# Performance work log

Hardware: AMD Instinct MI355X
Metric: run time of the kernel (lower is better)

The kernel has to match this reference:

```python
import jax, jax.numpy as jnp
import numpy as np

DIM = 1024
NUM_HEADS = 16
HEAD_DIM = DIM // NUM_HEADS
PATCH_SIZE = 20
SHIFT = 2
B, N = 8, 4096


def _patch_index(n, patch_size, shift):
    """Replicates the torch module's static index construction (numpy, host-side)."""
    base = np.arange(0, patch_size * shift, shift, dtype=np.int64)[None, :]  # [1, ps]
    group = np.concatenate([base + i for i in range(shift)], axis=0)        # [shift, ps]
    blocks = [group]
    idx = group
    while idx[-1, -1] < n:
        idx = idx + patch_size * shift
        blocks.append(idx)
    return np.concatenate(blocks, axis=0)  # [R, ps], a permutation of 0..padded-1


PATCH_INDEX = _patch_index(N, PATCH_SIZE, SHIFT)
PAD_SIZE = PATCH_SIZE * SHIFT - N % (PATCH_SIZE * SHIFT)


def setup_inputs() -> dict:
    key = jax.random.key(0)
    k1, k2, k3 = jax.random.split(key, 3)
    x = jax.random.normal(k1, (B, N, DIM), dtype=jnp.float32)
    Wqkv = jax.random.normal(k2, (3 * DIM, DIM), dtype=jnp.float32) * 0.02  # torch Linear weight [out,in]
    Wout = jax.random.normal(k3, (DIM, DIM), dtype=jnp.float32) * 0.02
    bout = jnp.zeros((DIM,), dtype=jnp.float32)
    return {"x": x, "Wqkv": Wqkv, "Wout": Wout, "bout": bout}


def reference(x, Wqkv, Wout, bout):
    Bq, Nq, C = x.shape
    scale = HEAD_DIM ** -0.5
    pidx = jnp.asarray(PATCH_INDEX)                              # [R, S]
    x_pad = jnp.concatenate(
        [x, jnp.zeros((Bq, PAD_SIZE, C), dtype=x.dtype)], axis=1)  # [B, Np, C]
    xp = x_pad[:, pidx, :]                                        # gather -> [B, R, S, C]
    qkv = jnp.einsum('brsc,dc->brsd', xp, Wqkv)                   # [B, R, S, 3C]
    Rr, Sp = pidx.shape
    qkv = qkv.reshape(Bq, Rr, Sp, 3, NUM_HEADS, HEAD_DIM)
    q = qkv[..., 0, :, :].transpose(0, 1, 3, 2, 4)                # [B, R, H, S, hd]
    k = qkv[..., 1, :, :].transpose(0, 1, 3, 2, 4)
    v = qkv[..., 2, :, :].transpose(0, 1, 3, 2, 4)
    dots = jnp.einsum('brhsd,brhtd->brhst', q, k) * scale         # [B, R, H, S, S]
    attn = jax.nn.softmax(dots, axis=-1)                          # dropout: eval mode (identity)
    out = jnp.einsum('brhst,brhtd->brhsd', attn, v)               # [B, R, H, S, hd]
    out = out.transpose(0, 1, 3, 2, 4).reshape(Bq, Rr, Sp, C)
    # scatter back (patch_index is a permutation, so no conflicts)
    x_pad = x_pad.at[:, pidx.reshape(-1), :].set(out.reshape(Bq, -1, C))
    return x_pad[:, :Nq, :] @ Wout.T + bout
```

## Files before the change

### kernel.cpp

```cpp
#include <hip/hip_runtime.h>

#define BQ      8
#define SEQ     4096
#define DIM_    1024
#define QKVD    3072
#define NPATCH  206
#define MTOT    (BQ * SEQ)

typedef __bf16 bf16x8 __attribute__((ext_vector_type(8)));
typedef float  f32x4  __attribute__((ext_vector_type(4)));

__device__ __forceinline__ float bf2f(unsigned int u16) {
  union { unsigned int i; float f; } x;
  x.i = u16 << 16;
  return x.f;
}
__device__ __forceinline__ unsigned short f2bf(float f) {
  union { float f; unsigned int i; } x; x.f = f;
  unsigned int r = x.i + 0x7fffu + ((x.i >> 16) & 1u);
  return (unsigned short)(r >> 16);
}

__device__ __forceinline__ void load_lds16(const void* g, void* l) {
  __builtin_amdgcn_global_load_lds(
      (const __attribute__((address_space(1))) void*)g,
      (__attribute__((address_space(3))) void*)l, 16, 0, 0);
}

__global__ __launch_bounds__(256) void cvt_kernel(
    const float* __restrict__ x,  unsigned short* __restrict__ xb,
    const float* __restrict__ w1, unsigned short* __restrict__ w1b,
    const float* __restrict__ w2, unsigned short* __restrict__ w2b)
{
  const long long NX  = (long long)MTOT * DIM_;
  const long long NW1 = (long long)QKVD * DIM_;
  const long long NW2 = (long long)DIM_ * DIM_;
  const long long total4 = (NX + NW1 + NW2) >> 2;
  for (long long q = (long long)blockIdx.x * 256 + threadIdx.x; q < total4;
       q += (long long)gridDim.x * 256) {
    const float* src; unsigned short* dst; long long i;
    if (q < (NX >> 2))              { src = x;  dst = xb;  i = (q << 2); }
    else if (q < ((NX + NW1) >> 2)) { src = w1; dst = w1b; i = (q << 2) - NX; }
    else                            { src = w2; dst = w2b; i = (q << 2) - NX - NW1; }
    float4 v = *(const float4*)(src + i);
    ushort4 o;
    o.x = f2bf(v.x); o.y = f2bf(v.y); o.z = f2bf(v.z); o.w = f2bf(v.w);
    *(ushort4*)(dst + i) = o;
  }
}

#define MFMA_Q(IH, JH)                                                        \
  _Pragma("unroll") for (int i_ = 0; i_ < 4; ++i_)                            \
  _Pragma("unroll") for (int j_ = 0; j_ < 2; ++j_) {                          \
    acc[(IH)*4 + i_][(JH)*2 + j_] = __builtin_amdgcn_mfma_f32_16x16x32_bf16(  \
        af[IH][i_][0], bf_[j_][0], acc[(IH)*4 + i_][(JH)*2 + j_], 0, 0, 0);   \
    acc[(IH)*4 + i_][(JH)*2 + j_] = __builtin_amdgcn_mfma_f32_16x16x32_bf16(  \
        af[IH][i_][1], bf_[j_][1], acc[(IH)*4 + i_][(JH)*2 + j_], 0, 0, 0);   \
  }

#define STAGE_A(H, KT, BUF) do {                                              \
    const int kof_ = (KT) * 64;                                               \
    unsigned short* d_ = &lds[(BUF) * 32768 + (H) * 8192 + tid * 8];          \
    load_lds16(a_src0 + (size_t)(H) * 128 * K + kof_, d_);                    \
    load_lds16(a_src1 + (size_t)(H) * 128 * K + kof_, d_ + 4096);             \
  } while (0)

#define STAGE_B(H, KT, BUF) do {                                              \
    const int kof_ = (KT) * 64;                                               \
    unsigned short* d_ = &lds[(BUF) * 32768 + 16384 + (H) * 8192 + tid * 8];  \
    load_lds16(b_src0 + (size_t)(H) * 128 * K + kof_, d_);                    \
    load_lds16(b_src1 + (size_t)(H) * 128 * K + kof_, d_ + 4096);             \
  } while (0)

#define OPEN_BARRIER  __builtin_amdgcn_s_barrier()
#define CLOSE_BARRIER asm volatile("s_barrier" ::: "memory")
#define WAIT_LGKM0    asm volatile("s_waitcnt lgkmcnt(0)" ::: "memory")

template <bool HAS_BIAS, bool OUT_F32>
__global__ __launch_bounds__(512, 2) void gemm_bt256(
    const unsigned short* __restrict__ A,
    const unsigned short* __restrict__ Bm,
    const float* __restrict__ bias,
    void* __restrict__ Cv,
    int N, int K)
{
  __shared__ alignas(16) unsigned short lds[2 * 32768];

  const int tid  = threadIdx.x;
  const int wave = tid >> 6;
  const int lane = tid & 63;
  const int wr = wave >> 2;
  const int wc = wave & 3;
  const int fr = lane & 15;
  const int fq = lane >> 4;
  const size_t bm = (size_t)blockIdx.y * 256;
  const size_t bn = (size_t)blockIdx.x * 256;

  int r_s[2], c_s[2];
#pragma unroll
  for (int p = 0; p < 2; ++p) {
    int byte = (p * 512 + tid) * 16;
    int lo = byte ^ (((byte >> 7) & 7) << 4);
    r_s[p] = lo >> 7;
    c_s[p] = (lo & 127) >> 1;
  }
  const unsigned short* a_src0 = A  + (bm + r_s[0]) * (size_t)K + c_s[0];
  const unsigned short* a_src1 = A  + (bm + r_s[1]) * (size_t)K + c_s[1];
  const unsigned short* b_src0 = Bm + (bn + r_s[0]) * (size_t)K + c_s[0];
  const unsigned short* b_src1 = Bm + (bn + r_s[1]) * (size_t)K + c_s[1];

  const int offu0 = ((fr * 128 +  0 + fq * 16) ^ ((fr & 7) << 4)) >> 1;
  const int offu1 = ((fr * 128 + 64 + fq * 16) ^ ((fr & 7) << 4)) >> 1;
  const int awo = wr * 8192;
  const int bwo = 16384 + (wc >> 1) * 8192 + (wc & 1) * 4096;

  f32x4 acc[8][4];
#pragma unroll
  for (int i = 0; i < 8; ++i)
#pragma unroll
    for (int j = 0; j < 4; ++j)
      acc[i][j] = (f32x4){0.f, 0.f, 0.f, 0.f};

  const int NT = K >> 6;

  STAGE_B(0, 0, 0); STAGE_B(1, 0, 0);
  STAGE_A(0, 0, 0); STAGE_A(1, 0, 0);
  STAGE_A(0, 1, 1); STAGE_A(1, 1, 1);
  asm volatile("s_waitcnt vmcnt(4)" ::: "memory");
  __builtin_amdgcn_s_barrier();

  bf16x8 af[2][4][2];
  bf16x8 bf_[2][2];

  for (int T = 0; T < NT; ++T) {
    const int cur = T & 1;
    const unsigned short* bufc = &lds[cur * 32768];
    const int ktB = (T + 1 < NT) ? T + 1 : NT - 1;
    const int ktA = (T + 2 < NT) ? T + 2 : NT - 1;

#pragma unroll
    for (int i = 0; i < 4; ++i) {
      af[0][i][0] = *(const bf16x8*)&bufc[awo + i * 1024 + offu0];
      af[0][i][1] = *(const bf16x8*)&bufc[awo + i * 1024 + offu1];
    }
#pragma unroll
    for (int j = 0; j < 2; ++j) {
      bf_[j][0] = *(const bf16x8*)&bufc[bwo + j * 1024 + offu0];
      bf_[j][1] = *(const bf16x8*)&bufc[bwo + j * 1024 + offu1];
    }
    STAGE_B(0, ktB, cur ^ 1);
    OPEN_BARRIER;
    WAIT_LGKM0;
    __builtin_amdgcn_s_setprio(1);
    MFMA_Q(0, 0)
    __builtin_amdgcn_s_setprio(0);
    CLOSE_BARRIER;

#pragma unroll
    for (int i = 0; i < 4; ++i) {
      af[1][i][0] = *(const bf16x8*)&bufc[awo + 4096 + i * 1024 + offu0];
      af[1][i][1] = *(const bf16x8*)&bufc[awo + 4096 + i * 1024 + offu1];
    }
    STAGE_B(1, ktB, cur ^ 1);
    OPEN_BARRIER;
    WAIT_LGKM0;
    __builtin_amdgcn_s_setprio(1);
    MFMA_Q(1, 0)
    __builtin_amdgcn_s_setprio(0);
    CLOSE_BARRIER;

#pragma unroll
    for (int j = 0; j < 2; ++j) {
      bf_[j][0] = *(const bf16x8*)&bufc[bwo + 2048 + j * 1024 + offu0];
      bf_[j][1] = *(const bf16x8*)&bufc[bwo + 2048 + j * 1024 + offu1];
    }
    STAGE_A(0, ktA, cur);
    OPEN_BARRIER;
    WAIT_LGKM0;
    __builtin_amdgcn_s_setprio(1);
    MFMA_Q(0, 1)
    __builtin_amdgcn_s_setprio(0);
    CLOSE_BARRIER;

    STAGE_A(1, ktA, cur);
    OPEN_BARRIER;
    __builtin_amdgcn_s_setprio(1);
    MFMA_Q(1, 1)
    __builtin_amdgcn_s_setprio(0);
    asm volatile("s_waitcnt vmcnt(4)" ::: "memory");
    CLOSE_BARRIER;
  }

  const int crow0 = fq * 4;
  const int ccol  = fr;
  float bv[4];
  if (HAS_BIAS) {
#pragma unroll
    for (int j = 0; j < 4; ++j) bv[j] = bias[bn + wc * 64 + j * 16 + ccol];
  }
#pragma unroll
  for (int i = 0; i < 8; ++i) {
#pragma unroll
    for (int j = 0; j < 4; ++j) {
      size_t base = (bm + wr * 128 + i * 16 + crow0) * (size_t)N
                  + (bn + wc * 64 + j * 16 + ccol);
#pragma unroll
      for (int r2 = 0; r2 < 4; ++r2) {
        float v = acc[i][j][r2];
        if (HAS_BIAS) v += bv[j];
        if (OUT_F32) ((float*)Cv)[base + (size_t)r2 * N] = v;
        else ((unsigned short*)Cv)[base + (size_t)r2 * N] = f2bf(v);
      }
    }
  }
}

#define KSF 516
#define VST 520
__global__ __launch_bounds__(256) void attn_kernel(
    const unsigned short* __restrict__ qkv,
    unsigned short* __restrict__ y)
{
  const int r    = blockIdx.x;
  const int half = blockIdx.y;
  const int b    = blockIdx.z;
  const int tid  = threadIdx.x;
  const int tbase = 40 * (r >> 1) + (r & 1);
  const int hq_off = half * 512;

  __shared__ alignas(16) float Ksf[20 * KSF];
  __shared__ alignas(16) unsigned short Vs[20 * VST];
  __shared__ float L[8 * 20 * 20];

  for (int c = tid; c < 2560; c += 256) {
    int tok = c >> 7;
    int kv  = (c >> 6) & 1;
    int j   = c & 63;
    int t   = tbase + 2 * tok;
    int4 data;
    if (t < SEQ) {
      const unsigned short* src = qkv + ((size_t)(b * SEQ + t)) * QKVD
                                  + 1024 + kv * 1024 + hq_off + j * 8;
      data = *(const int4*)src;
    } else {
      data = make_int4(0, 0, 0, 0);
    }
    if (kv == 0) {
      const unsigned short* u = (const unsigned short*)&data;
      float4 f0, f1;
      f0.x = bf2f(u[0]); f0.y = bf2f(u[1]); f0.z = bf2f(u[2]); f0.w = bf2f(u[3]);
      f1.x = bf2f(u[4]); f1.y = bf2f(u[5]); f1.z = bf2f(u[6]); f1.w = bf2f(u[7]);
      *(float4*)(&Ksf[tok * KSF + j * 8])     = f0;
      *(float4*)(&Ksf[tok * KSF + j * 8 + 4]) = f1;
    } else {
      *(int4*)(&Vs[tok * VST + j * 8]) = data;
    }
  }
  __syncthreads();

  for (int i = tid; i < 3200; i += 256) {
    int h   = i / 400;
    int rem = i - h * 400;
    int s   = rem / 20;
    int u   = rem - s * 20;
    int tq  = tbase + 2 * s;
    float dot = 0.f;
    if (tq < SEQ) {
      const int2* q64 = (const int2*)(qkv + (size_t)(b * SEQ + tq) * QKVD + hq_off + h * 64);
      const f32x4* kf = (const f32x4*)(&Ksf[u * KSF + h * 64]);
#pragma unroll
      for (int e4 = 0; e4 < 16; ++e4) {
        int2 qa = q64[e4];
        f32x4 kv4 = kf[e4];
        dot += bf2f((unsigned int)qa.x & 0xffffu) * kv4.x
             + bf2f((unsigned int)qa.x >> 16)     * kv4.y
             + bf2f((unsigned int)qa.y & 0xffffu) * kv4.z
             + bf2f((unsigned int)qa.y >> 16)     * kv4.w;
      }
    }
    L[(h * 20 + s) * 20 + u] = dot * 0.125f;
  }
  __syncthreads();

  if (tid < 160) {
    int h = tid / 20;
    int s = tid - h * 20;
    float* row = &L[(h * 20 + s) * 20];
    float m = -1e30f;
#pragma unroll
    for (int u = 0; u < 20; ++u) m = fmaxf(m, row[u]);
    float w[20];
    float sum = 0.f;
#pragma unroll
    for (int u = 0; u < 20; ++u) { w[u] = __expf(row[u] - m); sum += w[u]; }
    float inv = 1.f / sum;
#pragma unroll
    for (int u = 0; u < 20; ++u) row[u] = w[u] * inv;
  }
  __syncthreads();

  for (int i = tid; i < 2560; i += 256) {
    int e4   = i & 15;
    int rest = i >> 4;
    int s    = rest % 20;
    int h    = rest / 20;
    int tq   = tbase + 2 * s;
    if (tq >= SEQ) continue;
    const float* w = &L[(h * 20 + s) * 20];
    const unsigned short* vp = Vs + h * 64 + e4 * 4;
    float a0 = 0.f, a1 = 0.f, a2 = 0.f, a3 = 0.f;
#pragma unroll
    for (int u = 0; u < 20; ++u) {
      float wu = w[u];
      uint2 vv = *(const uint2*)(vp + u * VST);
      a0 += wu * bf2f(vv.x & 0xffffu);
      a1 += wu * bf2f(vv.x >> 16);
      a2 += wu * bf2f(vv.y & 0xffffu);
      a3 += wu * bf2f(vv.y >> 16);
    }
    ushort4 o;
    o.x = f2bf(a0); o.y = f2bf(a1); o.z = f2bf(a2); o.w = f2bf(a3);
    *(ushort4*)(&y[(size_t)(b * SEQ + tq) * DIM_ + hq_off + h * 64 + e4 * 4]) = o;
  }
}

extern "C" void kernel_launch(void* const* d_in, const int* in_sizes, int n_in,
                              void* d_out, int out_size, void* d_ws, size_t ws_size,
                              hipStream_t stream) {
  const float* x    = (const float*)d_in[0];
  const float* Wqkv = (const float*)d_in[1];
  const float* Wout = (const float*)d_in[2];
  const float* bout = (const float*)d_in[3];
  float* out = (float*)d_out;

  unsigned short* xb_y  = (unsigned short*)d_ws;
  unsigned short* wqkvb = xb_y  + (size_t)MTOT * DIM_;
  unsigned short* woutb = wqkvb + (size_t)QKVD * DIM_;
  unsigned short* qkv   = woutb + (size_t)DIM_ * DIM_;

  cvt_kernel<<<2048, 256, 0, stream>>>(x, xb_y, Wqkv, wqkvb, Wout, woutb);

  gemm_bt256<false, false><<<dim3(QKVD / 256, MTOT / 256), 512, 0, stream>>>(
      xb_y, wqkvb, nullptr, qkv, QKVD, DIM_);

  attn_kernel<<<dim3(NPATCH, 2, BQ), 256, 0, stream>>>(qkv, xb_y);

  gemm_bt256<true, true><<<dim3(DIM_ / 256, MTOT / 256), 512, 0, stream>>>(
      xb_y, woutb, bout, out, DIM_, DIM_);
}
```

Baseline: 661.2 us.

## Use a 128x128-tile GEMM kernel for the output projection

Adds a simpler 128x128-tile, 256-thread bf16 MFMA GEMM with bias and fp32 output, and uses it for the output projection instead of the 256x256 pipelined kernel. The 256 kernel is specialised to bf16 output without bias. The intent is more blocks and better CU balance for the N=1024 GEMM. In exchange the new kernel loses double buffering and software pipelining, adds two barriers per K step, and reuses less data per tile.

Result: slower. 709.2 us (+7.3%).

```diff
diff --git a/kernel.cpp b/kernel.cpp
--- a/kernel.cpp
+++ b/kernel.cpp
@@ -76,11 +76,9 @@
 #define CLOSE_BARRIER asm volatile("s_barrier" ::: "memory")
 #define WAIT_LGKM0    asm volatile("s_waitcnt lgkmcnt(0)" ::: "memory")
 
-template <bool HAS_BIAS, bool OUT_F32>
 __global__ __launch_bounds__(512, 2) void gemm_bt256(
     const unsigned short* __restrict__ A,
     const unsigned short* __restrict__ Bm,
-    const float* __restrict__ bias,
     void* __restrict__ Cv,
     int N, int K)
 {
@@ -193,17 +191,98 @@
 
   const int crow0 = fq * 4;
   const int ccol  = fr;
-  float bv[4];
-  if (HAS_BIAS) {
-#pragma unroll
-    for (int j = 0; j < 4; ++j) bv[j] = bias[bn + wc * 64 + j * 16 + ccol];
-  }
 #pragma unroll
   for (int i = 0; i < 8; ++i) {
 #pragma unroll
     for (int j = 0; j < 4; ++j) {
       size_t base = (bm + wr * 128 + i * 16 + crow0) * (size_t)N
                   + (bn + wc * 64 + j * 16 + ccol);
+#pragma unroll
+      for (int r2 = 0; r2 < 4; ++r2) {
+        ((unsigned short*)Cv)[base + (size_t)r2 * N] = f2bf(acc[i][j][r2]);
+      }
+    }
+  }
+}
+
+template <bool HAS_BIAS, bool OUT_F32>
+__global__ __launch_bounds__(256) void gemm_bt128(
+    const unsigned short* __restrict__ A,
+    const unsigned short* __restrict__ Bm,
+    const float* __restrict__ bias,
+    void* __restrict__ Cv,
+    int N, int K)
+{
+  __shared__ alignas(16) unsigned short As[128 * 32];
+  __shared__ alignas(16) unsigned short Bs[128 * 32];
+
+  const int tid  = threadIdx.x;
+  const size_t bm = (size_t)blockIdx.y * 128;
+  const size_t bn = (size_t)blockIdx.x * 128;
+  const int wave = tid >> 6;
+  const int lane = tid & 63;
+  const int wm = (wave >> 1) * 64;
+  const int wn = (wave & 1) * 64;
+  const int fr = lane & 15;
+  const int fq = lane >> 4;
+
+  f32x4 acc[4][4];
+#pragma unroll
+  for (int i = 0; i < 4; ++i)
+#pragma unroll
+    for (int j = 0; j < 4; ++j)
+      acc[i][j] = (f32x4){0.f, 0.f, 0.f, 0.f};
+
+  const int srow  = tid >> 2;
+  const int c_src = (tid & 3) ^ ((tid >> 3) & 3);
+  const int scol  = c_src * 8;
+  const unsigned short* gA0 = A  + (bm + srow) * (size_t)K + scol;
+  const unsigned short* gA1 = A  + (bm + 64 + srow) * (size_t)K + scol;
+  const unsigned short* gB0 = Bm + (bn + srow) * (size_t)K + scol;
+  const unsigned short* gB1 = Bm + (bn + 64 + srow) * (size_t)K + scol;
+  unsigned short* lA0 = &As[tid * 8];
+  unsigned short* lA1 = &As[2048 + tid * 8];
+  unsigned short* lB0 = &Bs[tid * 8];
+  unsigned short* lB1 = &Bs[2048 + tid * 8];
+
+  const int frx = fr * 32 + ((fq ^ ((fr >> 1) & 3)) * 8);
+  const int ga0 = ((wm >> 4) + 0) * 512 + frx;
+  const int gb0 = ((wn >> 4) + 0) * 512 + frx;
+
+  for (int kt = 0; kt < K; kt += 32) {
+    load_lds16(gA0 + kt, lA0);
+    load_lds16(gA1 + kt, lA1);
+    load_lds16(gB0 + kt, lB0);
+    load_lds16(gB1 + kt, lB1);
+    __syncthreads();
+
+    bf16x8 af[4], bfm[4];
+#pragma unroll
+    for (int i = 0; i < 4; ++i)
+      af[i] = *(const bf16x8*)(&As[ga0 + i * 512]);
+#pragma unroll
+    for (int j = 0; j < 4; ++j)
+      bfm[j] = *(const bf16x8*)(&Bs[gb0 + j * 512]);
+#pragma unroll
+    for (int i = 0; i < 4; ++i)
+#pragma unroll
+      for (int j = 0; j < 4; ++j)
+        acc[i][j] = __builtin_amdgcn_mfma_f32_16x16x32_bf16(af[i], bfm[j], acc[i][j], 0, 0, 0);
+    __syncthreads();
+  }
+
+  const int crow0 = (lane >> 4) * 4;
+  const int ccol  = lane & 15;
+  float bv[4];
+  if (HAS_BIAS) {
+#pragma unroll
+    for (int j = 0; j < 4; ++j) bv[j] = bias[bn + wn + j * 16 + ccol];
+  }
+#pragma unroll
+  for (int i = 0; i < 4; ++i) {
+#pragma unroll
+    for (int j = 0; j < 4; ++j) {
+      size_t base = (bm + wm + i * 16 + crow0) * (size_t)N + (bn + wn + j * 16 + ccol);
 #pragma unroll
       for (int r2 = 0; r2 < 4; ++r2) {
         float v = acc[i][j][r2];
@@ -340,11 +419,11 @@
 
   cvt_kernel<<<2048, 256, 0, stream>>>(x, xb_y, Wqkv, wqkvb, Wout, woutb);
 
-  gemm_bt256<false, false><<<dim3(QKVD / 256, MTOT / 256), 512, 0, stream>>>(
-      xb_y, wqkvb, nullptr, qkv, QKVD, DIM_);
+  gemm_bt256<<<dim3(QKVD / 256, MTOT / 256), 512, 0, stream>>>(
+      xb_y, wqkvb, qkv, QKVD, DIM_);
 
   attn_kernel<<<dim3(NPATCH, 2, BQ), 256, 0, stream>>>(qkv, xb_y);
 
-  gemm_bt256<true, true><<<dim3(DIM_ / 256, MTOT / 256), 512, 0, stream>>>(
+  gemm_bt128<true, true><<<dim3(DIM_ / 128, MTOT / 128), 256, 0, stream>>>(
       xb_y, woutb, bout, out, DIM_, DIM_);
 }
```

## Rewrite patch attention kernel with per-wave MFMA for QK^T and PV

Applied to the files above, without the earlier changes.

Replaces the scalar LDS-based attention (fp32 K staging, per-thread dot products, separate softmax pass and scalar PV) with a per-wave design: each wave owns two heads and computes QK^T and P·V using bf16 16x16x32 MFMA instructions, with the softmax done in registers via lane shuffles. The 20-token patch is padded to 32 with masking. Block-wide barriers are removed and shared memory is reorganised per wave, with occupancy hinted to 3 blocks per CU. This targets the ALU-bound scalar attention stage, at the cost of padding waste and bf16 rounding of the unnormalised probabilities.

After: 576.8 us. 1.15x faster.

```diff
diff --git a/kernel.cpp b/kernel.cpp
--- a/kernel.cpp
+++ b/kernel.cpp
@@ -215,112 +215,155 @@
   }
 }
 
-#define KSF 516
-#define VST 520
-__global__ __launch_bounds__(256) void attn_kernel(
+#define VHS 2120
+#define PWS 2048
+#define WSZ (2*VHS + PWS)
+__global__ __launch_bounds__(256, 3) void attn_kernel(
     const unsigned short* __restrict__ qkv,
     unsigned short* __restrict__ y)
 {
+  __shared__ alignas(16) unsigned short SM[4 * WSZ];
+
   const int r    = blockIdx.x;
   const int half = blockIdx.y;
   const int b    = blockIdx.z;
   const int tid  = threadIdx.x;
+  const int wave = tid >> 6;
+  const int lane = tid & 63;
+  const int fq   = lane >> 4;
+  const int fr   = lane & 15;
   const int tbase = 40 * (r >> 1) + (r & 1);
-  const int hq_off = half * 512;
-
-  __shared__ alignas(16) float Ksf[20 * KSF];
-  __shared__ alignas(16) unsigned short Vs[20 * VST];
-  __shared__ float L[8 * 20 * 20];
-
-  for (int c = tid; c < 2560; c += 256) {
-    int tok = c >> 7;
-    int kv  = (c >> 6) & 1;
-    int j   = c & 63;
-    int t   = tbase + 2 * tok;
-    int4 data;
+  const int hq   = half * 512;
+  const size_t rowB = (size_t)b * SEQ;
+
+  unsigned short* W  = &SM[wave * WSZ];
+  unsigned short* Ps = W + 2 * VHS;
+
+  const int ulim = (SEQ - tbase + 1) >> 1;
+
+  const int4 z4 = make_int4(0, 0, 0, 0);
+  for (int z = lane; z < (2 * VHS) / 8; z += 64) *(int4*)(W + z * 8) = z4;
+  for (int z = lane; z < PWS / 8; z += 64)       *(int4*)(Ps + z * 8) = z4;
+
+  for (int c = lane; c < 320; c += 64) {
+    int u  = c >> 4;
+    int hl = (c >> 3) & 1;
+    int d8 = c & 7;
+    int t  = tbase + 2 * u;
     if (t < SEQ) {
-      const unsigned short* src = qkv + ((size_t)(b * SEQ + t)) * QKVD
-                                  + 1024 + kv * 1024 + hq_off + j * 8;
-      data = *(const int4*)src;
-    } else {
-      data = make_int4(0, 0, 0, 0);
-    }
-    if (kv == 0) {
-      const unsigned short* u = (const unsigned short*)&data;
-      float4 f0, f1;
-      f0.x = bf2f(u[0]); f0.y = bf2f(u[1]); f0.z = bf2f(u[2]); f0.w = bf2f(u[3]);
-      f1.x = bf2f(u[4]); f1.y = bf2f(u[5]); f1.z = bf2f(u[6]); f1.w = bf2f(u[7]);
-      *(float4*)(&Ksf[tok * KSF + j * 8])     = f0;
-      *(float4*)(&Ksf[tok * KSF + j * 8 + 4]) = f1;
-    } else {
-      *(int4*)(&Vs[tok * VST + j * 8]) = data;
-    }
-  }
-  __syncthreads();
-
-  for (int i = tid; i < 3200; i += 256) {
-    int h   = i / 400;
-    int rem = i - h * 400;
-    int s   = rem / 20;
-    int u   = rem - s * 20;
-    int tq  = tbase + 2 * s;
-    float dot = 0.f;
-    if (tq < SEQ) {
-      const int2* q64 = (const int2*)(qkv + (size_t)(b * SEQ + tq) * QKVD + hq_off + h * 64);
-      const f32x4* kf = (const f32x4*)(&Ksf[u * KSF + h * 64]);
-#pragma unroll
-      for (int e4 = 0; e4 < 16; ++e4) {
-        int2 qa = q64[e4];
-        f32x4 kv4 = kf[e4];
-        dot += bf2f((unsigned int)qa.x & 0xffffu) * kv4.x
-             + bf2f((unsigned int)qa.x >> 16)     * kv4.y
-             + bf2f((unsigned int)qa.y & 0xffffu) * kv4.z
-             + bf2f((unsigned int)qa.y >> 16)     * kv4.w;
+      const unsigned short* src = qkv + (rowB + t) * (size_t)QKVD
+                                  + 2048 + hq + (wave * 2 + hl) * 64 + d8 * 8;
+      int4 v = *(const int4*)src;
+      unsigned short* dst = W + hl * VHS + u * 66 + d8 * 8;
+      *(unsigned int*)(dst)     = (unsigned int)v.x;
+      *(unsigned int*)(dst + 2) = (unsigned int)v.y;
+      *(unsigned int*)(dst + 4) = (unsigned int)v.z;
+      *(unsigned int*)(dst + 6) = (unsigned int)v.w;
+    }
+  }
+
+  int tok0 = tbase + 2 * fr;          if (tok0 > SEQ - 1) tok0 = SEQ - 1;
+  int tok1 = tbase + 2 * (16 + fr);   if (tok1 > SEQ - 1) tok1 = SEQ - 1;
+  const unsigned short* row0 = qkv + (rowB + tok0) * (size_t)QKVD;
+  const unsigned short* row1 = qkv + (rowB + tok1) * (size_t)QKVD;
+
+#pragma unroll
+  for (int hl = 0; hl < 2; ++hl) {
+    const int ho = hq + (wave * 2 + hl) * 64;
+
+    bf16x8 aQ[2][2], bK[2][2];
+#pragma unroll
+    for (int kk = 0; kk < 2; ++kk) {
+      aQ[0][kk] = *(const bf16x8*)(row0 + ho + kk * 32 + fq * 8);
+      aQ[1][kk] = *(const bf16x8*)(row1 + ho + kk * 32 + fq * 8);
+      bK[0][kk] = *(const bf16x8*)(row0 + 1024 + ho + kk * 32 + fq * 8);
+      bK[1][kk] = *(const bf16x8*)(row1 + 1024 + ho + kk * 32 + fq * 8);
+    }
+
+    f32x4 acc[2][2];
+#pragma unroll
+    for (int m = 0; m < 2; ++m)
+#pragma unroll
+      for (int n = 0; n < 2; ++n)
+        acc[m][n] = (f32x4){0.f, 0.f, 0.f, 0.f};
+#pragma unroll
+    for (int kk = 0; kk < 2; ++kk)
+#pragma unroll
+      for (int m = 0; m < 2; ++m)
+#pragma unroll
+        for (int n = 0; n < 2; ++n)
+          acc[m][n] = __builtin_amdgcn_mfma_f32_16x16x32_bf16(
+              aQ[m][kk], bK[n][kk], acc[m][n], 0, 0, 0);
+
+    float ex0[2][4], ex1[2][4], inv_[2][4];
+    const bool u1v = (fr < 4);
+#pragma unroll
+    for (int m = 0; m < 2; ++m) {
+#pragma unroll
+      for (int q2 = 0; q2 < 4; ++q2) {
+        float v0 = acc[m][0][q2] * 0.125f;
+        float v1 = acc[m][1][q2] * 0.125f;
+        if (fr >= ulim) v0 = 0.f;
+        if (16 + fr >= ulim) v1 = 0.f;
+        float mx = u1v ? fmaxf(v0, v1) : v0;
+        mx = fmaxf(mx, __shfl_xor(mx, 1));
+        mx = fmaxf(mx, __shfl_xor(mx, 2));
+        mx = fmaxf(mx, __shfl_xor(mx, 4));
+        mx = fmaxf(mx, __shfl_xor(mx, 8));
+        float e0 = __expf(v0 - mx);
+        float e1 = u1v ? __expf(v1 - mx) : 0.f;
+        float sm = e0 + e1;
+        sm += __shfl_xor(sm, 1);
+        sm += __shfl_xor(sm, 2);
+        sm += __shfl_xor(sm, 4);
+        sm += __shfl_xor(sm, 8);
+        ex0[m][q2] = e0; ex1[m][q2] = e1;
+        inv_[m][q2] = 1.f / sm;
       }
     }
-    L[(h * 20 + s) * 20 + u] = dot * 0.125f;
-  }
-  __syncthreads();
-
-  if (tid < 160) {
-    int h = tid / 20;
-    int s = tid - h * 20;
-    float* row = &L[(h * 20 + s) * 20];
-    float m = -1e30f;
-#pragma unroll
-    for (int u = 0; u < 20; ++u) m = fmaxf(m, row[u]);
-    float w[20];
-    float sum = 0.f;
-#pragma unroll
-    for (int u = 0; u < 20; ++u) { w[u] = __expf(row[u] - m); sum += w[u]; }
-    float inv = 1.f / sum;
-#pragma unroll
-    for (int u = 0; u < 20; ++u) row[u] = w[u] * inv;
-  }
-  __syncthreads();
-
-  for (int i = tid; i < 2560; i += 256) {
-    int e4   = i & 15;
-    int rest = i >> 4;
-    int s    = rest % 20;
-    int h    = rest / 20;
-    int tq   = tbase + 2 * s;
-    if (tq >= SEQ) continue;
-    const float* w = &L[(h * 20 + s) * 20];
-    const unsigned short* vp = Vs + h * 64 + e4 * 4;
-    float a0 = 0.f, a1 = 0.f, a2 = 0.f, a3 = 0.f;
-#pragma unroll
-    for (int u = 0; u < 20; ++u) {
-      float wu = w[u];
-      uint2 vv = *(const uint2*)(vp + u * VST);
-      a0 += wu * bf2f(vv.x & 0xffffu);
-      a1 += wu * bf2f(vv.x >> 16);
-      a2 += wu * bf2f(vv.y & 0xffffu);
-      a3 += wu * bf2f(vv.y >> 16);
-    }
-    ushort4 o;
-    o.x = f2bf(a0); o.y = f2bf(a1); o.z = f2bf(a2); o.w = f2bf(a3);
-    *(ushort4*)(&y[(size_t)(b * SEQ + tq) * DIM_ + hq_off + h * 64 + e4 * 4]) = o;
+
+#pragma unroll
+    for (int m = 0; m < 2; ++m) {
+      unsigned short* pb = Ps + (hl * 2 + m) * 512;
+#pragma unroll
+      for (int q2 = 0; q2 < 4; ++q2) {
+        pb[((fr >> 3) * 16 + fq * 4 + q2) * 8 + (fr & 7)] = f2bf(ex0[m][q2]);
+        if (u1v) pb[(32 + fq * 4 + q2) * 8 + fr] = f2bf(ex1[m][q2]);
+      }
+    }
+
+    bf16x8 pA[2];
+#pragma unroll
+    for (int m = 0; m < 2; ++m)
+      pA[m] = *(const bf16x8*)(Ps + (hl * 2 + m) * 512 + lane * 8);
+
+    f32x4 o[2][4];
+#pragma unroll
+    for (int n = 0; n < 4; ++n) {
+      union { unsigned short s[8]; bf16x8 v; } g;
+#pragma unroll
+      for (int j = 0; j < 8; ++j)
+        g.s[j] = W[hl * VHS + (fq * 8 + j) * 66 + n * 16 + fr];
+#pragma unroll
+      for (int m = 0; m < 2; ++m)
+        o[m][n] = __builtin_amdgcn_mfma_f32_16x16x32_bf16(
+            pA[m], g.v, (f32x4){0.f, 0.f, 0.f, 0.f}, 0, 0, 0);
+    }
+
+#pragma unroll
+    for (int m = 0; m < 2; ++m) {
+#pragma unroll
+      for (int q2 = 0; q2 < 4; ++q2) {
+        int s = m * 16 + fq * 4 + q2;
+        int t = tbase + 2 * s;
+        if (s < 20 && t < SEQ) {
+          size_t yb = (rowB + t) * (size_t)DIM_ + ho;
+#pragma unroll
+          for (int n = 0; n < 4; ++n)
+            y[yb + n * 16 + fr] = f2bf(o[m][n][q2] * inv_[m][q2]);
+        }
+      }
+    }
   }
 }
 
```
